# Optimization experiments

Measured on AMD Instinct MI355X. Metric: run time of the kernel, lower is better.

The kernel has to match this reference:

```python
import jax, jax.numpy as jnp
import numpy as np

B, N, C, H, D = 1, 256, 128, 4, 32  # batch, n_res, c_z, heads, head_dim
LN_EPS = 1e-5


def setup_inputs() -> dict:
    key = jax.random.key(0)
    ks = jax.random.split(key, 10)
    s = 0.02
    return {
        "act": jax.random.normal(ks[0], (B, N, N, C), dtype=jnp.float32),
        "mask": jnp.ones((B, N, N), dtype=jnp.float32),
        "ln_g": jnp.ones((C,), dtype=jnp.float32),
        "ln_b": jnp.zeros((C,), dtype=jnp.float32),
        "w2d": jax.random.normal(ks[1], (C, H), dtype=jnp.float32) * s,
        "wq": jax.random.normal(ks[2], (C, H, D), dtype=jnp.float32) * s,
        "wk": jax.random.normal(ks[3], (C, H, D), dtype=jnp.float32) * s,
        "wv": jax.random.normal(ks[4], (C, H, D), dtype=jnp.float32) * s,
        "wg": jax.random.normal(ks[5], (C, H, D), dtype=jnp.float32) * s,
        "bg": jnp.ones((H, D), dtype=jnp.float32),
        "wo": jax.random.normal(ks[6], (H, D, C), dtype=jnp.float32) * s,
        "bo": jnp.zeros((C,), dtype=jnp.float32),
    }


def reference(act, mask, ln_g, ln_b, w2d, wq, wk, wv, wg, bg, wo, bo):
    # LayerNorm over channel dim
    mu = jnp.mean(act, axis=-1, keepdims=True)
    var = jnp.mean(jnp.square(act - mu), axis=-1, keepdims=True)
    x = (act - mu) * jax.lax.rsqrt(var + LN_EPS) * ln_g + ln_b  # [B,N,N,C]

    # mask bias: [B, I, 1, 1, K]
    mask_bias = (1e9 * (mask - 1.0))[:, :, None, None, :]
    # nonbatched pair bias: [B, 1, H, Q, K]
    nb_bias = jnp.einsum('bqkc,ch->bhqk', x, w2d)[:, None]

    scale = 1.0 / jnp.sqrt(jnp.asarray(D, dtype=x.dtype))
    q = jnp.einsum('bijc,chd->bijhd', x, wq) * scale  # [B,I,Q,H,D]
    k = jnp.einsum('bijc,chd->bijhd', x, wk)
    v = jnp.einsum('bijc,chd->bijhd', x, wv)

    logits = jnp.einsum('biqhd,bikhd->bihqk', q, k) + mask_bias + nb_bias
    a = jax.nn.softmax(logits, axis=-1)  # [B,I,H,Q,K]
    o = jnp.einsum('bihqk,bikhd->biqhd', a, v)  # [B,I,Q,H,D]

    g = jax.nn.sigmoid(jnp.einsum('bijc,chd->bijhd', x, wg) + bg)
    o = o * g
    out = jnp.einsum('biqhd,hdc->biqc', o, wo) + bo  # [B,N,N,C]
    return out
```

## Files before the change

### kernel.cpp

```cpp
#include <hip/hip_runtime.h>

#define QK_SCALE 0.17677669529663689f

typedef float f4 __attribute__((ext_vector_type(4)));
typedef short bf16x8 __attribute__((ext_vector_type(8)));
typedef float f32x4 __attribute__((ext_vector_type(4)));
typedef unsigned short us4 __attribute__((ext_vector_type(4)));
typedef unsigned int u32x2 __attribute__((ext_vector_type(2)));

__device__ __forceinline__ unsigned short f2bf(float x){
  unsigned int u = __float_as_uint(x);
  u += 0x7fffu + ((u >> 16) & 1u);
  return (unsigned short)(u >> 16);
}
__device__ __forceinline__ float bf2f(unsigned short h){
  return __uint_as_float(((unsigned int)h) << 16);
}
__device__ __forceinline__ unsigned int cvtpk(float lo, float hi){
  unsigned int r;
  asm volatile("v_cvt_pk_bf16_f32 %0, %1, %2" : "=v"(r) : "v"(lo), "v"(hi));
  return r;
}
__device__ __forceinline__ f32x4 mfma16(bf16x8 a, bf16x8 b, f32x4 c){
  return __builtin_amdgcn_mfma_f32_16x16x32_bf16(a, b, c, 0, 0, 0);
}
__device__ __forceinline__ void gload_lds16(const void* g, void* s){
  __builtin_amdgcn_global_load_lds(
      (const __attribute__((address_space(1))) unsigned int*)g,
      (__attribute__((address_space(3))) unsigned int*)s, 16, 0, 0);
}

__global__ __launch_bounds__(256)
void k_prep(const float* __restrict__ wq, const float* __restrict__ wk,
            const float* __restrict__ wv, const float* __restrict__ wg,
            const float* __restrict__ wo, unsigned short* __restrict__ pk)
{
  const int m = blockIdx.x;
  const float* W = (m==0)? wq : (m==1)? wk : (m==2)? wv : (m==3)? wg : wo;
  const float scale = (m==0)? QK_SCALE : 1.0f;
  unsigned short* dst = pk + (long)m * 32768;
  for (int ent = threadIdx.x; ent < 2048; ent += 256){
    const int l = ent & 63, ktn = ent >> 6;
    const int kt = ktn & 3, nt = ktn >> 2;
    unsigned short* ph = dst + ((nt*4 + kt)*2 + 0)*512 + l*8;
    unsigned short* pl = dst + ((nt*4 + kt)*2 + 1)*512 + l*8;
    #pragma unroll
    for (int e = 0; e < 8; ++e){
      const int row = kt*32 + (l>>4)*8 + e;
      const int col = nt*16 + (l&15);
      float v = W[row*128 + col] * scale;
      unsigned short hh = f2bf(v);
      ph[e] = hh;
      pl[e] = f2bf(v - bf2f(hh));
    }
  }
}

__global__ __launch_bounds__(512, 4)
void k_proj(const float* __restrict__ act, const float* __restrict__ ln_g,
            const float* __restrict__ ln_b, const float* __restrict__ w2d,
            const unsigned short* __restrict__ pk, const float* __restrict__ bg,
            unsigned short* __restrict__ qf, unsigned short* __restrict__ kf,
            unsigned short* __restrict__ vt, unsigned short* __restrict__ gg,
            float* __restrict__ b2d)
{
  __shared__ unsigned short afr[8*4*2*512];
  __shared__ unsigned short sc[4*640];
  const int t = threadIdx.x, w = t>>6, l = t&63, g16 = l>>4, c = l&15;
  const long p0 = (long)blockIdx.x * 128;
  const int bi = (int)(p0 >> 8);
  const int qb0 = (int)(p0 & 255);
  const int row = w*16 + c;

  {
    const float* ap = act + (p0 + row)*128;
    f4 xv[4][2];
    #pragma unroll
    for (int kt = 0; kt < 4; ++kt){
      xv[kt][0] = *(const f4*)(ap + kt*32 + g16*8);
      xv[kt][1] = *(const f4*)(ap + kt*32 + g16*8 + 4);
    }
    float s = 0.f, s2 = 0.f;
    #pragma unroll
    for (int kt = 0; kt < 4; ++kt)
      #pragma unroll
      for (int u = 0; u < 2; ++u)
        #pragma unroll
        for (int e = 0; e < 4; ++e){
          float x = xv[kt][u][e]; s += x; s2 += x*x;
        }
    s += __shfl_xor(s,16); s2 += __shfl_xor(s2,16);
    s += __shfl_xor(s,32); s2 += __shfl_xor(s2,32);
    const float mu = s*(1.f/128.f);
    const float iv = rsqrtf(fmaxf(s2*(1.f/128.f)-mu*mu,0.f)+1e-5f);

    float pb0=0.f, pb1=0.f, pb2=0.f, pb3=0.f;
    #pragma unroll
    for (int kt = 0; kt < 4; ++kt){
      bf16x8 hv, lv;
      #pragma unroll
      for (int u = 0; u < 2; ++u){
        const int cb = kt*32 + g16*8 + u*4;
        f4 lg = *(const f4*)(ln_g + cb);
        f4 lb = *(const f4*)(ln_b + cb);
        #pragma unroll
        for (int e0 = 0; e0 < 4; ++e0){
          float vv = (xv[kt][u][e0]-mu)*iv*lg[e0] + lb[e0];
          f4 wp = *(const f4*)(w2d + (cb+e0)*4);
          pb0 += vv*wp[0]; pb1 += vv*wp[1]; pb2 += vv*wp[2]; pb3 += vv*wp[3];
          unsigned short hh = f2bf(vv);
          hv[u*4+e0] = (short)hh;
          lv[u*4+e0] = (short)f2bf(vv - bf2f(hh));
        }
      }
      *(bf16x8*)&afr[((w*4+kt)*2+0)*512 + l*8] = hv;
      *(bf16x8*)&afr[((w*4+kt)*2+1)*512 + l*8] = lv;
    }
    pb0 += __shfl_xor(pb0,16); pb1 += __shfl_xor(pb1,16);
    pb2 += __shfl_xor(pb2,16); pb3 += __shfl_xor(pb3,16);
    pb0 += __shfl_xor(pb0,32); pb1 += __shfl_xor(pb1,32);
    pb2 += __shfl_xor(pb2,32); pb3 += __shfl_xor(pb3,32);
    const float pbsel = (g16==0)? pb0 : (g16==1)? pb1 : (g16==2)? pb2 : pb3;
    b2d[g16*65536 + (int)p0 + row] = pbsel;
  }
  __syncthreads();

  #pragma unroll
  for (int pass = 0; pass < 2; ++pass){
    bf16x8 bh0[4], bl0[4], bh1[4], bl1[4];
    { const int ntg = w*4 + pass*2;
      #pragma unroll
      for (int kt = 0; kt < 4; ++kt){
        bh0[kt] = *(const bf16x8*)(pk + ((ntg*4+kt)*2+0)*512 + l*8);
        bl0[kt] = *(const bf16x8*)(pk + ((ntg*4+kt)*2+1)*512 + l*8);
        bh1[kt] = *(const bf16x8*)(pk + (((ntg+1)*4+kt)*2+0)*512 + l*8);
        bl1[kt] = *(const bf16x8*)(pk + (((ntg+1)*4+kt)*2+1)*512 + l*8);
      } }
    for (int rt = 0; rt < 8; ++rt){
      bf16x8 ah[4], al[4];
      #pragma unroll
      for (int kt = 0; kt < 4; ++kt){
        ah[kt] = *(const bf16x8*)&afr[((rt*4+kt)*2+0)*512 + l*8];
        al[kt] = *(const bf16x8*)&afr[((rt*4+kt)*2+1)*512 + l*8];
      }
      f32x4 a0 = {0.f,0.f,0.f,0.f}, a1 = {0.f,0.f,0.f,0.f};
      #pragma unroll
      for (int kt = 0; kt < 4; ++kt){
        a0 = mfma16(ah[kt], bh0[kt], a0);
        a1 = mfma16(ah[kt], bh1[kt], a1);
        a0 = mfma16(ah[kt], bl0[kt], a0);
        a1 = mfma16(ah[kt], bl1[kt], a1);
        a0 = mfma16(al[kt], bh0[kt], a0);
        a1 = mfma16(al[kt], bh1[kt], a1);
      }
      if (w < 4){
        unsigned short* scw = sc + w*640;
        #pragma unroll
        for (int j = 0; j < 4; ++j){
          scw[(g16*4+j)*40 + c]      = f2bf(a0[j]);
          scw[(g16*4+j)*40 + 16 + c] = f2bf(a1[j]);
        }
        asm volatile("" ::: "memory");
        bf16x8 fr = *(const bf16x8*)&scw[c*40 + g16*8];
        const int head = (w&1)*2 + pass;
        unsigned short* dst = (w < 2) ? qf : kf;
        *(bf16x8*)&dst[(((long)bi*4+head)*16 + (qb0>>4) + rt)*512 + l*8] = fr;
        asm volatile("" ::: "memory");
      } else if (w < 6){
        const int ntv0 = (w-4)*4 + pass*2;
        const int kv = qb0 + rt*16 + g16*4;
        #pragma unroll
        for (int np = 0; np < 2; ++np){
          const int colg = (ntv0+np)*16 + c;
          const int head = colg >> 5, d = colg & 31;
          f32x4 aa = np ? a1 : a0;
          us4 v4;
          #pragma unroll
          for (int j = 0; j < 4; ++j) v4[j] = f2bf(aa[j]);
          const int vb = (d*512 + kv*2) ^ ((d&7)<<4);
          *(us4*)((char*)vt + ((long)bi*4+head)*16384 + vb) = v4;
        }
      } else {
        const int colb = (w-6)*64 + pass*32;
        const int row0 = (int)p0 + rt*16 + g16*4;
        const float bg0 = bg[colb + c];
        const float bg1 = bg[colb + 16 + c];
        #pragma unroll
        for (int j = 0; j < 4; ++j){
          float g0 = 1.f/(1.f + __expf(-(a0[j] + bg0)));
          float g1 = 1.f/(1.f + __expf(-(a1[j] + bg1)));
          gg[(row0+j)*128 + colb + c]      = f2bf(g0);
          gg[(row0+j)*128 + colb + 16 + c] = f2bf(g1);
        }
      }
    }
  }
}

__global__ __launch_bounds__(512, 4)
void k_attn(const unsigned short* __restrict__ qf, const unsigned short* __restrict__ kfg,
            const unsigned short* __restrict__ vt, const unsigned short* __restrict__ gg,
            const float* __restrict__ b2d, const float* __restrict__ mask,
            unsigned short* __restrict__ obf)
{
  __shared__ unsigned short k_s[16*512];
  __shared__ unsigned short v_s[8192];
  __shared__ unsigned short p_s[8*1024];
  __shared__ float mb_s[256];
  const int t = threadIdx.x, w = t>>6, l = t&63, g16 = l>>4, c = l&15;
  const int bi = blockIdx.x >> 2, h = blockIdx.x & 3;
  const int base = (bi*4+h)*8192;

  #pragma unroll
  for (int cc = 0; cc < 4; ++cc){
    const int ch = w*4 + cc;
    if (ch < 16) gload_lds16(kfg + base + ch*512 + l*8, k_s + ch*512);
    else         gload_lds16(vt + base + (ch-16)*512 + l*8, v_s + (ch-16)*512);
  }
  if (t < 256) mb_s[t] = 1e9f * (mask[bi*256 + t] - 1.0f);
  asm volatile("s_waitcnt vmcnt(0)" ::: "memory");
  __syncthreads();

  char* pw = (char*)(p_s + w*1024);
  const int swz = (c&7)<<4;

  for (int im = 0; im < 2; ++im){
    const int q0 = w*32 + im*16;
    const bf16x8 qfr = *(const bf16x8*)(qf + base + (q0>>4)*512 + l*8);
    const float* bq = b2d + h*65536 + (q0 + c)*256 + g16*4;
    f32x4 sa[16];
    #pragma unroll
    for (int nt = 0; nt < 16; ++nt){
      f4 bv = *(const f4*)(bq + nt*16);
      f4 mv = *(const f4*)&mb_s[nt*16 + g16*4];
      f32x4 ci;
      ci[0]=bv[0]+mv[0]; ci[1]=bv[1]+mv[1]; ci[2]=bv[2]+mv[2]; ci[3]=bv[3]+mv[3];
      sa[nt] = mfma16(*(const bf16x8*)(k_s + nt*512 + l*8), qfr, ci);
    }
    float mx = fmaxf(fmaxf(sa[0][0], sa[0][1]), fmaxf(sa[0][2], sa[0][3]));
    #pragma unroll
    for (int nt = 1; nt < 16; ++nt)
      mx = fmaxf(mx, fmaxf(fmaxf(sa[nt][0], sa[nt][1]), fmaxf(sa[nt][2], sa[nt][3])));
    mx = fmaxf(mx, __shfl_xor(mx, 16));
    mx = fmaxf(mx, __shfl_xor(mx, 32));
    const float nmx = -mx * 1.44269504f;
    float sum = 0.f;
    #pragma unroll
    for (int nt = 0; nt < 16; ++nt){
      #pragma unroll
      for (int j = 0; j < 4; ++j){
        float e = exp2f(fmaf(sa[nt][j], 1.44269504f, nmx));
        sa[nt][j] = e; sum += e;
      }
    }
    sum += __shfl_xor(sum, 16);
    sum += __shfl_xor(sum, 32);
    const float inv = 1.f / sum;
    f32x4 oa0 = {0.f,0.f,0.f,0.f}, oa1 = {0.f,0.f,0.f,0.f};
    #pragma unroll
    for (int p4 = 0; p4 < 4; ++p4){
      #pragma unroll
      for (int ntl = 0; ntl < 4; ++ntl){
        const int nt = p4*4 + ntl;
        u32x2 pk2;
        pk2[0] = cvtpk(sa[nt][0], sa[nt][1]);
        pk2[1] = cvtpk(sa[nt][2], sa[nt][3]);
        *(u32x2*)(pw + c*128 + ((ntl*32 + g16*8) ^ swz)) = pk2;
      }
      asm volatile("s_waitcnt lgkmcnt(0)" ::: "memory");
      __builtin_amdgcn_sched_barrier(0);
      #pragma unroll
      for (int ktl = 0; ktl < 2; ++ktl){
        const int kt = p4*2 + ktl;
        bf16x8 pf = *(const bf16x8*)(pw + c*128 + ((ktl*64 + g16*16) ^ swz));
        const int vb0 = ((c*512      + kt*64 + g16*16) ^ swz);
        const int vb1 = (((16+c)*512 + kt*64 + g16*16) ^ swz);
        oa0 = mfma16(*(const bf16x8*)((const char*)v_s + vb0), pf, oa0);
        oa1 = mfma16(*(const bf16x8*)((const char*)v_s + vb1), pf, oa1);
      }
      asm volatile("" ::: "memory");
      __builtin_amdgcn_sched_barrier(0);
    }
    const int row = bi*256 + q0 + c;
    us4 gv0 = *(const us4*)&gg[row*128 + h*32 + g16*4];
    us4 gv1 = *(const us4*)&gg[row*128 + h*32 + 16 + g16*4];
    u32x2 o0, o1;
    o0[0] = cvtpk(oa0[0]*inv*bf2f(gv0[0]), oa0[1]*inv*bf2f(gv0[1]));
    o0[1] = cvtpk(oa0[2]*inv*bf2f(gv0[2]), oa0[3]*inv*bf2f(gv0[3]));
    o1[0] = cvtpk(oa1[0]*inv*bf2f(gv1[0]), oa1[1]*inv*bf2f(gv1[1]));
    o1[1] = cvtpk(oa1[2]*inv*bf2f(gv1[2]), oa1[3]*inv*bf2f(gv1[3]));
    *(u32x2*)&obf[row*128 + h*32 + g16*4]      = o0;
    *(u32x2*)&obf[row*128 + h*32 + 16 + g16*4] = o1;
  }
}

__global__ __launch_bounds__(512, 4)
void k_out(const unsigned short* __restrict__ obf, const unsigned short* __restrict__ pko,
           const float* __restrict__ bo, float* __restrict__ out)
{
  __shared__ unsigned short afr[32*512];
  const int t = threadIdx.x, w = t>>6, l = t&63, g16 = l>>4, c = l&15;
  const long p0 = (long)blockIdx.x * 128;

  #pragma unroll
  for (int u = 0; u < 4; ++u){
    const int pr = w*4 + u;
    const int rt = pr >> 2, kt = pr & 3;
    gload_lds16(obf + (p0 + rt*16 + c)*128 + kt*32 + g16*8, afr + pr*512);
  }
  asm volatile("s_waitcnt vmcnt(0)" ::: "memory");
  __syncthreads();

  bf16x8 bh[4], bl[4];
  #pragma unroll
  for (int kt = 0; kt < 4; ++kt){
    bh[kt] = *(const bf16x8*)(pko + ((w*4+kt)*2+0)*512 + l*8);
    bl[kt] = *(const bf16x8*)(pko + ((w*4+kt)*2+1)*512 + l*8);
  }
  const float bov = bo[w*16 + c];
  for (int rt = 0; rt < 8; ++rt){
    f32x4 a0 = {bov, bov, bov, bov};
    #pragma unroll
    for (int kt = 0; kt < 4; ++kt){
      bf16x8 af = *(const bf16x8*)&afr[(rt*4+kt)*512 + l*8];
      a0 = mfma16(af, bh[kt], a0);
      a0 = mfma16(af, bl[kt], a0);
    }
    const int row0 = (int)p0 + rt*16 + g16*4;
    #pragma unroll
    for (int j = 0; j < 4; ++j)
      out[(row0+j)*128 + w*16 + c] = a0[j];
  }
}

extern "C" void kernel_launch(void* const* d_in, const int* in_sizes, int n_in,
                              void* d_out, int out_size, void* d_ws, size_t ws_size,
                              hipStream_t stream) {
  const float* act  = (const float*)d_in[0];
  const float* mask = (const float*)d_in[1];
  const float* ln_g = (const float*)d_in[2];
  const float* ln_b = (const float*)d_in[3];
  const float* w2d  = (const float*)d_in[4];
  const float* wq   = (const float*)d_in[5];
  const float* wk   = (const float*)d_in[6];
  const float* wv   = (const float*)d_in[7];
  const float* wg   = (const float*)d_in[8];
  const float* bg   = (const float*)d_in[9];
  const float* wo   = (const float*)d_in[10];
  const float* bo   = (const float*)d_in[11];
  float* out = (float*)d_out;

  char* ws = (char*)d_ws;
  unsigned short* qf  = (unsigned short*)(ws);
  unsigned short* kfb = (unsigned short*)(ws + 16777216L);
  unsigned short* vt  = (unsigned short*)(ws + 33554432L);
  unsigned short* gg  = (unsigned short*)(ws + 50331648L);
  unsigned short* obf = (unsigned short*)(ws + 67108864L);
  float* b2d = (float*)(ws + 83886080L);
  unsigned short* pk = (unsigned short*)(ws + 84934656L);

  k_prep<<<5, 256, 0, stream>>>(wq, wk, wv, wg, wo, pk);
  k_proj<<<512, 512, 0, stream>>>(act, ln_g, ln_b, w2d, pk, bg,
                                  qf, kfb, vt, gg, b2d);
  k_attn<<<1024, 512, 0, stream>>>(qf, kfb, vt, gg, b2d, mask, obf);
  k_out<<<512, 512, 0, stream>>>(obf, pk + 4*32768, bo, out);
}
```

Baseline: 110.9 us.

## Store pair bias as bf16 and shuffle P in registers instead of LDS

The pair-bias tensor is now written and read as bf16 instead of fp32, which halves its traffic between the projection and attention kernels. In attention, the softmax probabilities are rearranged into the PV MFMA operand layout with ds_bpermute instead of a round trip through per-wave LDS scratch with waitcnt and sched barriers, so the p_s buffer is removed. Q fragments are loaded once before the main barrier, and the max and sum reductions use four independent lanes to shorten dependency chains. The bias loses precision from the bf16 rounding, and the bpermute lane mapping must exactly match the MFMA B-operand layout.

```diff
diff --git a/kernel.cpp b/kernel.cpp
--- a/kernel.cpp
+++ b/kernel.cpp
@@ -7,6 +7,7 @@
 typedef float f32x4 __attribute__((ext_vector_type(4)));
 typedef unsigned short us4 __attribute__((ext_vector_type(4)));
 typedef unsigned int u32x2 __attribute__((ext_vector_type(2)));
+typedef unsigned int u32x4 __attribute__((ext_vector_type(4)));
 
 __device__ __forceinline__ unsigned short f2bf(float x){
   unsigned int u = __float_as_uint(x);
@@ -62,7 +63,7 @@
             const unsigned short* __restrict__ pk, const float* __restrict__ bg,
             unsigned short* __restrict__ qf, unsigned short* __restrict__ kf,
             unsigned short* __restrict__ vt, unsigned short* __restrict__ gg,
-            float* __restrict__ b2d)
+            unsigned short* __restrict__ b2dh)
 {
   __shared__ unsigned short afr[8*4*2*512];
   __shared__ unsigned short sc[4*640];
@@ -121,7 +122,7 @@
     pb0 += __shfl_xor(pb0,32); pb1 += __shfl_xor(pb1,32);
     pb2 += __shfl_xor(pb2,32); pb3 += __shfl_xor(pb3,32);
     const float pbsel = (g16==0)? pb0 : (g16==1)? pb1 : (g16==2)? pb2 : pb3;
-    b2d[g16*65536 + (int)p0 + row] = pbsel;
+    b2dh[g16*65536 + (int)p0 + row] = f2bf(pbsel);
   }
   __syncthreads();
 
@@ -200,12 +201,11 @@
 __global__ __launch_bounds__(512, 4)
 void k_attn(const unsigned short* __restrict__ qf, const unsigned short* __restrict__ kfg,
             const unsigned short* __restrict__ vt, const unsigned short* __restrict__ gg,
-            const float* __restrict__ b2d, const float* __restrict__ mask,
+            const unsigned short* __restrict__ b2dh, const float* __restrict__ mask,
             unsigned short* __restrict__ obf)
 {
   __shared__ unsigned short k_s[16*512];
   __shared__ unsigned short v_s[8192];
-  __shared__ unsigned short p_s[8*1024];
   __shared__ float mb_s[256];
   const int t = threadIdx.x, w = t>>6, l = t&63, g16 = l>>4, c = l&15;
   const int bi = blockIdx.x >> 2, h = blockIdx.x & 3;
@@ -218,68 +218,84 @@
     else         gload_lds16(vt + base + (ch-16)*512 + l*8, v_s + (ch-16)*512);
   }
   if (t < 256) mb_s[t] = 1e9f * (mask[bi*256 + t] - 1.0f);
+  const bf16x8 qfr0 = *(const bf16x8*)(qf + base + (w*2+0)*512 + l*8);
+  const bf16x8 qfr1 = *(const bf16x8*)(qf + base + (w*2+1)*512 + l*8);
   asm volatile("s_waitcnt vmcnt(0)" ::: "memory");
   __syncthreads();
 
-  char* pw = (char*)(p_s + w*1024);
   const int swz = (c&7)<<4;
-
+  const int a0 = (((l & 16) << 1) | c) << 2;
+  const int a1 = a0 + 64;
+  const bool hi = (l >= 32);
+
+  #pragma unroll
   for (int im = 0; im < 2; ++im){
     const int q0 = w*32 + im*16;
-    const bf16x8 qfr = *(const bf16x8*)(qf + base + (q0>>4)*512 + l*8);
-    const float* bq = b2d + h*65536 + (q0 + c)*256 + g16*4;
+    const bf16x8 qfr = im ? qfr1 : qfr0;
+    const unsigned short* bq = b2dh + h*65536 + (q0 + c)*256 + g16*4;
     f32x4 sa[16];
     #pragma unroll
     for (int nt = 0; nt < 16; ++nt){
-      f4 bv = *(const f4*)(bq + nt*16);
-      f4 mv = *(const f4*)&mb_s[nt*16 + g16*4];
+      const us4 bh4 = *(const us4*)(bq + nt*16);
+      const f4 mv = *(const f4*)&mb_s[nt*16 + g16*4];
       f32x4 ci;
-      ci[0]=bv[0]+mv[0]; ci[1]=bv[1]+mv[1]; ci[2]=bv[2]+mv[2]; ci[3]=bv[3]+mv[3];
+      ci[0] = mv[0] + bf2f(bh4[0]);
+      ci[1] = mv[1] + bf2f(bh4[1]);
+      ci[2] = mv[2] + bf2f(bh4[2]);
+      ci[3] = mv[3] + bf2f(bh4[3]);
       sa[nt] = mfma16(*(const bf16x8*)(k_s + nt*512 + l*8), qfr, ci);
     }
-    float mx = fmaxf(fmaxf(sa[0][0], sa[0][1]), fmaxf(sa[0][2], sa[0][3]));
-    #pragma unroll
-    for (int nt = 1; nt < 16; ++nt)
-      mx = fmaxf(mx, fmaxf(fmaxf(sa[nt][0], sa[nt][1]), fmaxf(sa[nt][2], sa[nt][3])));
+    f32x4 mx4 = sa[0];
+    #pragma unroll
+    for (int nt = 1; nt < 16; ++nt){
+      mx4[0] = fmaxf(mx4[0], sa[nt][0]);
+      mx4[1] = fmaxf(mx4[1], sa[nt][1]);
+      mx4[2] = fmaxf(mx4[2], sa[nt][2]);
+      mx4[3] = fmaxf(mx4[3], sa[nt][3]);
+    }
+    float mx = fmaxf(fmaxf(mx4[0], mx4[1]), fmaxf(mx4[2], mx4[3]));
     mx = fmaxf(mx, __shfl_xor(mx, 16));
     mx = fmaxf(mx, __shfl_xor(mx, 32));
     const float nmx = -mx * 1.44269504f;
-    float sum = 0.f;
+    f32x4 sv = {0.f,0.f,0.f,0.f};
     #pragma unroll
     for (int nt = 0; nt < 16; ++nt){
       #pragma unroll
       for (int j = 0; j < 4; ++j){
         float e = exp2f(fmaf(sa[nt][j], 1.44269504f, nmx));
-        sa[nt][j] = e; sum += e;
-      }
-    }
+        sa[nt][j] = e;
+        sv[j] += e;
+      }
+    }
+    float sum = (sv[0]+sv[1]) + (sv[2]+sv[3]);
     sum += __shfl_xor(sum, 16);
     sum += __shfl_xor(sum, 32);
     const float inv = 1.f / sum;
     f32x4 oa0 = {0.f,0.f,0.f,0.f}, oa1 = {0.f,0.f,0.f,0.f};
     #pragma unroll
-    for (int p4 = 0; p4 < 4; ++p4){
-      #pragma unroll
-      for (int ntl = 0; ntl < 4; ++ntl){
-        const int nt = p4*4 + ntl;
-        u32x2 pk2;
-        pk2[0] = cvtpk(sa[nt][0], sa[nt][1]);
-        pk2[1] = cvtpk(sa[nt][2], sa[nt][3]);
-        *(u32x2*)(pw + c*128 + ((ntl*32 + g16*8) ^ swz)) = pk2;
-      }
-      asm volatile("s_waitcnt lgkmcnt(0)" ::: "memory");
-      __builtin_amdgcn_sched_barrier(0);
-      #pragma unroll
-      for (int ktl = 0; ktl < 2; ++ktl){
-        const int kt = p4*2 + ktl;
-        bf16x8 pf = *(const bf16x8*)(pw + c*128 + ((ktl*64 + g16*16) ^ swz));
-        const int vb0 = ((c*512      + kt*64 + g16*16) ^ swz);
-        const int vb1 = (((16+c)*512 + kt*64 + g16*16) ^ swz);
-        oa0 = mfma16(*(const bf16x8*)((const char*)v_s + vb0), pf, oa0);
-        oa1 = mfma16(*(const bf16x8*)((const char*)v_s + vb1), pf, oa1);
-      }
-      asm volatile("" ::: "memory");
-      __builtin_amdgcn_sched_barrier(0);
+    for (int kt = 0; kt < 8; ++kt){
+      const unsigned X0 = cvtpk(sa[2*kt][0],   sa[2*kt][1]);
+      const unsigned X1 = cvtpk(sa[2*kt][2],   sa[2*kt][3]);
+      const unsigned Y0 = cvtpk(sa[2*kt+1][0], sa[2*kt+1][1]);
+      const unsigned Y1 = cvtpk(sa[2*kt+1][2], sa[2*kt+1][3]);
+      const int pX0 = __builtin_amdgcn_ds_bpermute(a0, (int)X0);
+      const int pY0 = __builtin_amdgcn_ds_bpermute(a0, (int)Y0);
+      const int pX1 = __builtin_amdgcn_ds_bpermute(a0, (int)X1);
+      const int pY1 = __builtin_amdgcn_ds_bpermute(a0, (int)Y1);
+      const int pX2 = __builtin_amdgcn_ds_bpermute(a1, (int)X0);
+      const int pY2 = __builtin_amdgcn_ds_bpermute(a1, (int)Y0);
+      const int pX3 = __builtin_amdgcn_ds_bpermute(a1, (int)X1);
+      const int pY3 = __builtin_amdgcn_ds_bpermute(a1, (int)Y1);
+      u32x4 pu;
+      pu[0] = (unsigned)(hi ? pY0 : pX0);
+      pu[1] = (unsigned)(hi ? pY1 : pX1);
+      pu[2] = (unsigned)(hi ? pY2 : pX2);
+      pu[3] = (unsigned)(hi ? pY3 : pX3);
+      const bf16x8 pf = __builtin_bit_cast(bf16x8, pu);
+      const int vb0 = ((c*512      + kt*64 + g16*16) ^ swz);
+      const int vb1 = (((16+c)*512 + kt*64 + g16*16) ^ swz);
+      oa0 = mfma16(*(const bf16x8*)((const char*)v_s + vb0), pf, oa0);
+      oa1 = mfma16(*(const bf16x8*)((const char*)v_s + vb1), pf, oa1);
     }
     const int row = bi*256 + q0 + c;
     us4 gv0 = *(const us4*)&gg[row*128 + h*32 + g16*4];
@@ -351,17 +367,17 @@
   float* out = (float*)d_out;
 
   char* ws = (char*)d_ws;
-  unsigned short* qf  = (unsigned short*)(ws);
-  unsigned short* kfb = (unsigned short*)(ws + 16777216L);
-  unsigned short* vt  = (unsigned short*)(ws + 33554432L);
-  unsigned short* gg  = (unsigned short*)(ws + 50331648L);
-  unsigned short* obf = (unsigned short*)(ws + 67108864L);
-  float* b2d = (float*)(ws + 83886080L);
-  unsigned short* pk = (unsigned short*)(ws + 84934656L);
+  unsigned short* qf   = (unsigned short*)(ws);
+  unsigned short* kfb  = (unsigned short*)(ws + 16777216L);
+  unsigned short* vt   = (unsigned short*)(ws + 33554432L);
+  unsigned short* gg   = (unsigned short*)(ws + 50331648L);
+  unsigned short* obf  = (unsigned short*)(ws + 67108864L);
+  unsigned short* b2dh = (unsigned short*)(ws + 83886080L);
+  unsigned short* pk   = (unsigned short*)(ws + 84934656L);
 
   k_prep<<<5, 256, 0, stream>>>(wq, wk, wv, wg, wo, pk);
   k_proj<<<512, 512, 0, stream>>>(act, ln_g, ln_b, w2d, pk, bg,
-                                  qf, kfb, vt, gg, b2d);
-  k_attn<<<1024, 512, 0, stream>>>(qf, kfb, vt, gg, b2d, mask, obf);
+                                  qf, kfb, vt, gg, b2dh);
+  k_attn<<<1024, 512, 0, stream>>>(qf, kfb, vt, gg, b2dh, mask, obf);
   k_out<<<512, 512, 0, stream>>>(obf, pk + 4*32768, bo, out);
 }
```

Result: no change. 109.7 us (-1.1%).
